# Performance work log

Measured on AMD Instinct MI355X. Metric: run time of the kernel, lower is better.

The kernel has to match this reference:

```python
import jax, jax.numpy as jnp
import numpy as np

LMAX, RB, RA, N, D = 4, 12, 11, 131072, 64
S = (LMAX + 1) ** 2


def _assoc_legendre_norm(lmax, x):
    # Fully-normalized associated Legendre P_l^m(x), orthonormal over the sphere
    # (includes sqrt((2l+1)/(4pi) * (l-m)!/(l+m)!)). x: [B] = cos(beta).
    B = x.shape[0]
    s = np.sqrt(np.clip(1.0 - x * x, 0.0, 1.0))
    P = np.zeros((lmax + 1, lmax + 1, B))
    P[0, 0] = np.sqrt(1.0 / (4.0 * np.pi))
    for m in range(1, lmax + 1):
        P[m, m] = -np.sqrt((2.0 * m + 1.0) / (2.0 * m)) * s * P[m - 1, m - 1]
    for m in range(0, lmax):
        P[m + 1, m] = np.sqrt(2.0 * m + 3.0) * x * P[m, m]
    for m in range(0, lmax + 1):
        for l in range(m + 2, lmax + 1):
            a = np.sqrt((4.0 * l * l - 1.0) / (l * l - m * m))
            b = np.sqrt((((l - 1) ** 2 - m * m)) / (4.0 * (l - 1) ** 2 - 1.0))
            P[l, m] = a * (x * P[l - 1, m] - b * P[l - 2, m])
    return P


def _sh_grid(lmax, res_beta, res_alpha):
    # Real orthonormal spherical harmonics sampled on a Gauss-Legendre x uniform-alpha grid,
    # plus quadrature weights so that sum_{b,a} Y_i Y_j qw_b = delta_ij (band-limited).
    x, w = np.polynomial.legendre.leggauss(res_beta)  # nodes in cos(beta)
    alpha = 2.0 * np.pi * np.arange(res_alpha) / res_alpha
    P = _assoc_legendre_norm(lmax, x)  # [L+1, L+1, RB]
    Ssz = (lmax + 1) ** 2
    Y = np.zeros((res_beta, res_alpha, Ssz))
    i = 0
    for l in range(lmax + 1):
        for m in range(-l, l + 1):
            if m < 0:
                ang = np.sqrt(2.0) * np.sin(-m * alpha)
            elif m == 0:
                ang = np.ones_like(alpha)
            else:
                ang = np.sqrt(2.0) * np.cos(m * alpha)
            Y[:, :, i] = P[l, abs(m)][:, None] * ang[None, :]
            i += 1
    qw = w * (2.0 * np.pi / res_alpha)  # beta quadrature * alpha trapezoid weight
    return Y.astype(np.float32), qw.astype(np.float32)


def setup_inputs() -> dict:
    key = jax.random.key(0)
    k1, k2, k3, k4 = jax.random.split(key, 4)
    Y_np, qw_np = _sh_grid(LMAX, RB, RA)
    Y = jnp.asarray(Y_np)                       # [RB, RA, S]
    Yw = Y * jnp.asarray(qw_np)[:, None, None]  # [RB, RA, S] (quadrature-weighted)
    input1 = jax.random.normal(k1, (N, D), dtype=jnp.float32)
    input2 = jax.random.normal(k2, (N, D), dtype=jnp.float32)
    W1 = jax.random.normal(k3, (D, S), dtype=jnp.float32) * 0.1
    W2 = jax.random.normal(k4, (D, S), dtype=jnp.float32) * 0.1
    return {"input1": input1, "input2": input2, "W1": W1, "W2": W2, "Y": Y, "Yw": Yw}


def reference(input1, input2, W1, W2, Y, Yw):
    # linear_in: project input irreps to S2 spherical-harmonic coefficients
    c1 = input1 @ W1  # [N, S]
    c2 = input2 @ W2  # [N, S]
    # ToS2Grid: evaluate band-limited signal on the (beta, alpha) grid
    g1 = jnp.einsum("ns,bas->nba", c1, Y)  # [N, RB, RA]
    g2 = jnp.einsum("ns,bas->nba", c2, Y)
    # pointwise product on the sphere, then FromS2Grid (quadrature projection)
    return jnp.einsum("nba,bas->ns", g1 * g2, Yw)  # [N, S]
```

## Files before the change

kernel.cpp:

```cpp
#include <hip/hip_runtime.h>


typedef __bf16 bf16x8 __attribute__((ext_vector_type(8)));
typedef float f32x4 __attribute__((ext_vector_type(4)));

namespace {
constexpr int kD = 64, kS = 25, kP = 132;
constexpr int kBlock = 256, kM = 128;
constexpr int kHStride = 168;
constexpr int kSmemU = kM * kHStride;
constexpr int kWsA2 = 9216, kWsB2 = 18432;
}

__device__ __forceinline__ unsigned short f2bf(float f) {
    unsigned int u = __builtin_bit_cast(unsigned int, f);
    u += 0x7FFFu + ((u >> 16) & 1u);
    return (unsigned short)(u >> 16);
}

__device__ __forceinline__ bf16x8 ld_frag_g(const unsigned short* p) {
    int4 v = *reinterpret_cast<const int4*>(p);
    return __builtin_bit_cast(bf16x8, v);
}

__device__ __forceinline__ bf16x8 cvt8(f32x4 u, f32x4 v) {
    bf16x8 r;
    r[0] = (__bf16)u[0]; r[1] = (__bf16)u[1]; r[2] = (__bf16)u[2]; r[3] = (__bf16)u[3];
    r[4] = (__bf16)v[0]; r[5] = (__bf16)v[1]; r[6] = (__bf16)v[2]; r[7] = (__bf16)v[3];
    return r;
}

__global__ void precompute_kernel(const float* __restrict__ W1,
                                  const float* __restrict__ W2,
                                  const float* __restrict__ Y,
                                  const float* __restrict__ Yw,
                                  unsigned short* __restrict__ ws) {
    const int t0 = blockIdx.x * blockDim.x + threadIdx.x;
    const int stride = gridDim.x * blockDim.x;
    for (int e = t0; e < 9216; e += stride) {
        const int j = e & 7, lane = (e >> 3) & 63, ks = (e >> 9) & 1, nt = e >> 10;
        const int k = ks * 32 + (lane >> 4) * 8 + j;
        const int n = nt * 16 + (lane & 15);
        float v1 = 0.f, v2 = 0.f;
        if (n < kP) {
            const float* yr = Y + n * kS;
            const float* w1 = W1 + k * kS;
            const float* w2 = W2 + k * kS;
            #pragma unroll
            for (int s = 0; s < kS; ++s) {
                v1 = fmaf(w1[s], yr[s], v1);
                v2 = fmaf(w2[s], yr[s], v2);
            }
        }
        ws[e]         = f2bf(v1);
        ws[kWsA2 + e] = f2bf(v2);
    }
    for (int e = t0; e < 5120; e += stride) {
        const int j = e & 7, lane = (e >> 3) & 63, r = e >> 9;
        const int ks = r % 5, nt = r / 5;
        const int k = ks * 32 + (lane >> 4) * 8 + j;
        const int n = nt * 16 + (lane & 15);
        ws[kWsB2 + e] = (k < kP && n < kS) ? f2bf(Yw[k * kS + n]) : (unsigned short)0;
    }
}

__global__ __launch_bounds__(kBlock, 3) void gaunt_mfma5(
    const float* __restrict__ in1, const float* __restrict__ in2,
    const unsigned short* __restrict__ ws, float* __restrict__ out)
{
    __shared__ unsigned short smem[kSmemU];
    const int tid  = threadIdx.x;
    const int lane = tid & 63;
    const int w    = __builtin_amdgcn_readfirstlane(tid >> 6);
    const int lo16 = lane & 15, quad = lane >> 4;

    {
        const int r = tid >> 1, c = 144 + (tid & 1) * 8;
        *reinterpret_cast<int4*>(&smem[r * kHStride + c]) = (int4){0, 0, 0, 0};
    }

    const long long base = (long long)blockIdx.x * (kM * kD);
    bf16x8 a1f[2][2], a2f[2][2];
    #pragma unroll
    for (int rt = 0; rt < 2; ++rt) {
        const int row = (2 * w + rt) * 16 + lo16;
        const float* p1 = in1 + base + row * kD + quad * 8;
        const float* p2 = in2 + base + row * kD + quad * 8;
        #pragma unroll
        for (int ks = 0; ks < 2; ++ks) {
            const f32x4 u1 = *reinterpret_cast<const f32x4*>(p1 + ks * 32);
            const f32x4 v1 = *reinterpret_cast<const f32x4*>(p1 + ks * 32 + 4);
            const f32x4 u2 = *reinterpret_cast<const f32x4*>(p2 + ks * 32);
            const f32x4 v2 = *reinterpret_cast<const f32x4*>(p2 + ks * 32 + 4);
            a1f[rt][ks] = cvt8(u1, v1);
            a2f[rt][ks] = cvt8(u2, v2);
        }
    }

    const unsigned short* wsA1 = ws;
    const unsigned short* wsA2 = ws + kWsA2;
    bf16x8 b1c[2], b2c[2], b1n[2], b2n[2];
    #pragma unroll
    for (int ks = 0; ks < 2; ++ks) {
        b1c[ks] = ld_frag_g(&wsA1[ks * 512 + lane * 8]);
        b2c[ks] = ld_frag_g(&wsA2[ks * 512 + lane * 8]);
    }
    #pragma unroll 1
    for (int nt = 0; nt < 9; ++nt) {
        if (nt < 8) {
            #pragma unroll
            for (int ks = 0; ks < 2; ++ks) {
                b1n[ks] = ld_frag_g(&wsA1[((nt + 1) * 2 + ks) * 512 + lane * 8]);
                b2n[ks] = ld_frag_g(&wsA2[((nt + 1) * 2 + ks) * 512 + lane * 8]);
            }
        }
        #pragma unroll
        for (int rt = 0; rt < 2; ++rt) {
            f32x4 g1 = (f32x4){0.f, 0.f, 0.f, 0.f};
            f32x4 g2 = (f32x4){0.f, 0.f, 0.f, 0.f};
            #pragma unroll
            for (int ks = 0; ks < 2; ++ks) {
                g1 = __builtin_amdgcn_mfma_f32_16x16x32_bf16(a1f[rt][ks], b1c[ks], g1, 0, 0, 0);
                g2 = __builtin_amdgcn_mfma_f32_16x16x32_bf16(a2f[rt][ks], b2c[ks], g2, 0, 0, 0);
            }
            const int hcol = nt * 16 + lo16;
            #pragma unroll
            for (int i = 0; i < 4; ++i) {
                const int row = (2 * w + rt) * 16 + quad * 4 + i;
                smem[row * kHStride + hcol] =
                    __builtin_bit_cast(unsigned short, (__bf16)(g1[i] * g2[i]));
            }
        }
        #pragma unroll
        for (int ks = 0; ks < 2; ++ks) { b1c[ks] = b1n[ks]; b2c[ks] = b2n[ks]; }
    }

    const unsigned short* wsB2 = ws + kWsB2;
    f32x4 o[2][2];
    #pragma unroll
    for (int rt = 0; rt < 2; ++rt)
        #pragma unroll
        for (int nt = 0; nt < 2; ++nt)
            o[rt][nt] = (f32x4){0.f, 0.f, 0.f, 0.f};

    bf16x8 bbc[2], bbn[2];
    #pragma unroll
    for (int nt = 0; nt < 2; ++nt)
        bbc[nt] = ld_frag_g(&wsB2[(nt * 5) * 512 + lane * 8]);

    #pragma unroll 1
    for (int ks = 0; ks < 5; ++ks) {
        if (ks < 4) {
            #pragma unroll
            for (int nt = 0; nt < 2; ++nt)
                bbn[nt] = ld_frag_g(&wsB2[(nt * 5 + ks + 1) * 512 + lane * 8]);
        }
        bf16x8 hf[2];
        #pragma unroll
        for (int rt = 0; rt < 2; ++rt) {
            const int row = (2 * w + rt) * 16 + lo16;
            const int4 hv = *reinterpret_cast<const int4*>(
                &smem[row * kHStride + ks * 32 + quad * 8]);
            hf[rt] = __builtin_bit_cast(bf16x8, hv);
        }
        #pragma unroll
        for (int rt = 0; rt < 2; ++rt)
            #pragma unroll
            for (int nt = 0; nt < 2; ++nt)
                o[rt][nt] = __builtin_amdgcn_mfma_f32_16x16x32_bf16(
                    hf[rt], bbc[nt], o[rt][nt], 0, 0, 0);
        bbc[0] = bbn[0]; bbc[1] = bbn[1];
    }

    const long long ob = (long long)blockIdx.x * (kM * kS);
    #pragma unroll
    for (int rt = 0; rt < 2; ++rt) {
        #pragma unroll
        for (int nt = 0; nt < 2; ++nt) {
            const int col = nt * 16 + lo16;
            if (col < kS) {
                #pragma unroll
                for (int i = 0; i < 4; ++i) {
                    const int row = (2 * w + rt) * 16 + quad * 4 + i;
                    out[ob + row * kS + col] = o[rt][nt][i];
                }
            }
        }
    }
}

extern "C" void kernel_launch(void* const* d_in, const int* in_sizes, int n_in,
                              void* d_out, int out_size, void* d_ws, size_t ws_size,
                              hipStream_t stream) {
    const float* in1 = (const float*)d_in[0];
    const float* in2 = (const float*)d_in[1];
    const float* W1  = (const float*)d_in[2];
    const float* W2  = (const float*)d_in[3];
    const float* Y   = (const float*)d_in[4];
    const float* Yw  = (const float*)d_in[5];
    float* out = (float*)d_out;
    unsigned short* ws = (unsigned short*)d_ws;

    precompute_kernel<<<8, 256, 0, stream>>>(W1, W2, Y, Yw, ws);

    const int n_rows = in_sizes[0] / kD;
    const int grid = n_rows / kM;
    gaunt_mfma5<<<grid, kBlock, 0, stream>>>(in1, in2, ws, out);
}
```

Before: 118.0 us.

## Fuse grid product into projection MFMA via register transpose, drop LDS staging

The first GEMMs are computed transposed, with the grid points as rows and the sample rows as columns. The product g1*g2 therefore lands in registers already laid out as the B operand of a 16x16x16 f16 MFMA. That second projection now accumulates inside the same loop, removing the shared-memory buffer, its stores and loads, and the separate second phase. Precision moves from bf16 to fp16, occupancy hint rises to 4 blocks, and output stores are vectorized, at some risk of fp16 overflow or range issues.

```diff
diff --git a/kernel.cpp b/kernel.cpp
--- a/kernel.cpp
+++ b/kernel.cpp
@@ -1,86 +1,78 @@
 #include <hip/hip_runtime.h>
 
 
-typedef __bf16 bf16x8 __attribute__((ext_vector_type(8)));
+typedef _Float16 f16x8 __attribute__((ext_vector_type(8)));
+typedef _Float16 f16x4 __attribute__((ext_vector_type(4)));
 typedef float f32x4 __attribute__((ext_vector_type(4)));
+typedef float f32x4u __attribute__((ext_vector_type(4), aligned(4)));
 
 namespace {
 constexpr int kD = 64, kS = 25, kP = 132;
 constexpr int kBlock = 256, kM = 128;
-constexpr int kHStride = 168;
-constexpr int kSmemU = kM * kHStride;
-constexpr int kWsA2 = 9216, kWsB2 = 18432;
-}
-
-__device__ __forceinline__ unsigned short f2bf(float f) {
-    unsigned int u = __builtin_bit_cast(unsigned int, f);
-    u += 0x7FFFu + ((u >> 16) & 1u);
-    return (unsigned short)(u >> 16);
-}
-
-__device__ __forceinline__ bf16x8 ld_frag_g(const unsigned short* p) {
-    int4 v = *reinterpret_cast<const int4*>(p);
-    return __builtin_bit_cast(bf16x8, v);
-}
-
-__device__ __forceinline__ bf16x8 cvt8(f32x4 u, f32x4 v) {
-    bf16x8 r;
-    r[0] = (__bf16)u[0]; r[1] = (__bf16)u[1]; r[2] = (__bf16)u[2]; r[3] = (__bf16)u[3];
-    r[4] = (__bf16)v[0]; r[5] = (__bf16)v[1]; r[6] = (__bf16)v[2]; r[7] = (__bf16)v[3];
-    return r;
+constexpr int kWsA2 = 9216, kWsYw = 18432;
 }
 
 __global__ void precompute_kernel(const float* __restrict__ W1,
                                   const float* __restrict__ W2,
                                   const float* __restrict__ Y,
                                   const float* __restrict__ Yw,
-                                  unsigned short* __restrict__ ws) {
+                                  _Float16* __restrict__ ws) {
     const int t0 = blockIdx.x * blockDim.x + threadIdx.x;
     const int stride = gridDim.x * blockDim.x;
     for (int e = t0; e < 9216; e += stride) {
-        const int j = e & 7, lane = (e >> 3) & 63, ks = (e >> 9) & 1, nt = e >> 10;
-        const int k = ks * 32 + (lane >> 4) * 8 + j;
-        const int n = nt * 16 + (lane & 15);
+        const int j = e & 7, lane = (e >> 3) & 63, ks = (e >> 9) & 1, pt = e >> 10;
+        const int d = ks * 32 + (lane >> 4) * 8 + j;
+        const int p = pt * 16 + (lane & 15);
         float v1 = 0.f, v2 = 0.f;
-        if (n < kP) {
-            const float* yr = Y + n * kS;
-            const float* w1 = W1 + k * kS;
-            const float* w2 = W2 + k * kS;
+        if (p < kP) {
+            const float* yr = Y + p * kS;
+            const float* w1 = W1 + d * kS;
+            const float* w2 = W2 + d * kS;
             #pragma unroll
             for (int s = 0; s < kS; ++s) {
                 v1 = fmaf(w1[s], yr[s], v1);
                 v2 = fmaf(w2[s], yr[s], v2);
             }
         }
-        ws[e]         = f2bf(v1);
-        ws[kWsA2 + e] = f2bf(v2);
+        ws[e]         = (_Float16)v1;
+        ws[kWsA2 + e] = (_Float16)v2;
     }
-    for (int e = t0; e < 5120; e += stride) {
-        const int j = e & 7, lane = (e >> 3) & 63, r = e >> 9;
-        const int ks = r % 5, nt = r / 5;
-        const int k = ks * 32 + (lane >> 4) * 8 + j;
-        const int n = nt * 16 + (lane & 15);
-        ws[kWsB2 + e] = (k < kP && n < kS) ? f2bf(Yw[k * kS + n]) : (unsigned short)0;
+    for (int e = t0; e < 4608; e += stride) {
+        const int i = e & 3, lane = (e >> 2) & 63, r = e >> 8;
+        const int pt = r % 9, st = r / 9;
+        const int p = pt * 16 + ((lane >> 4) & 3) * 4 + i;
+        const int s = st * 16 + (lane & 15);
+        ws[kWsYw + e] = (s < kS && p < kP) ? (_Float16)Yw[p * kS + s]
+                                           : (_Float16)0.f;
     }
 }
 
-__global__ __launch_bounds__(kBlock, 3) void gaunt_mfma5(
+__device__ __forceinline__ f16x8 ld8(const _Float16* p) {
+    return *reinterpret_cast<const f16x8*>(p);
+}
+__device__ __forceinline__ f16x4 ld4(const _Float16* p) {
+    return *reinterpret_cast<const f16x4*>(p);
+}
+__device__ __forceinline__ f16x8 cvt8h(f32x4 u, f32x4 v) {
+    f16x8 r;
+    r[0] = (_Float16)u[0]; r[1] = (_Float16)u[1];
+    r[2] = (_Float16)u[2]; r[3] = (_Float16)u[3];
+    r[4] = (_Float16)v[0]; r[5] = (_Float16)v[1];
+    r[6] = (_Float16)v[2]; r[7] = (_Float16)v[3];
+    return r;
+}
+
+__global__ __launch_bounds__(kBlock, 4) void gaunt_mfma6(
     const float* __restrict__ in1, const float* __restrict__ in2,
-    const unsigned short* __restrict__ ws, float* __restrict__ out)
+    const _Float16* __restrict__ ws, float* __restrict__ out)
 {
-    __shared__ unsigned short smem[kSmemU];
     const int tid  = threadIdx.x;
     const int lane = tid & 63;
     const int w    = __builtin_amdgcn_readfirstlane(tid >> 6);
     const int lo16 = lane & 15, quad = lane >> 4;
 
-    {
-        const int r = tid >> 1, c = 144 + (tid & 1) * 8;
-        *reinterpret_cast<int4*>(&smem[r * kHStride + c]) = (int4){0, 0, 0, 0};
-    }
-
     const long long base = (long long)blockIdx.x * (kM * kD);
-    bf16x8 a1f[2][2], a2f[2][2];
+    f16x8 b1[2][2], b2[2][2];
     #pragma unroll
     for (int rt = 0; rt < 2; ++rt) {
         const int row = (2 * w + rt) * 16 + lo16;
@@ -92,27 +84,44 @@
             const f32x4 v1 = *reinterpret_cast<const f32x4*>(p1 + ks * 32 + 4);
             const f32x4 u2 = *reinterpret_cast<const f32x4*>(p2 + ks * 32);
             const f32x4 v2 = *reinterpret_cast<const f32x4*>(p2 + ks * 32 + 4);
-            a1f[rt][ks] = cvt8(u1, v1);
-            a2f[rt][ks] = cvt8(u2, v2);
+            b1[rt][ks] = cvt8h(u1, v1);
+            b2[rt][ks] = cvt8h(u2, v2);
         }
     }
 
-    const unsigned short* wsA1 = ws;
-    const unsigned short* wsA2 = ws + kWsA2;
-    bf16x8 b1c[2], b2c[2], b1n[2], b2n[2];
+    const _Float16* wsA1 = ws;
+    const _Float16* wsA2 = ws + kWsA2;
+    const _Float16* wsYw = ws + kWsYw;
+
+    f32x4 oacc[2][2];
+    #pragma unroll
+    for (int rt = 0; rt < 2; ++rt)
+        #pragma unroll
+        for (int st = 0; st < 2; ++st)
+            oacc[rt][st] = (f32x4){0.f, 0.f, 0.f, 0.f};
+
+    f16x8 a1c[2], a2c[2], a1n[2], a2n[2];
+    f16x4 ywc[2], ywn[2];
     #pragma unroll
     for (int ks = 0; ks < 2; ++ks) {
-        b1c[ks] = ld_frag_g(&wsA1[ks * 512 + lane * 8]);
-        b2c[ks] = ld_frag_g(&wsA2[ks * 512 + lane * 8]);
+        a1c[ks] = ld8(&wsA1[ks * 512 + lane * 8]);
+        a2c[ks] = ld8(&wsA2[ks * 512 + lane * 8]);
     }
+    #pragma unroll
+    for (int st = 0; st < 2; ++st)
+        ywc[st] = ld4(&wsYw[(st * 9) * 256 + lane * 4]);
+
     #pragma unroll 1
-    for (int nt = 0; nt < 9; ++nt) {
-        if (nt < 8) {
+    for (int pt = 0; pt < 9; ++pt) {
+        if (pt < 8) {
             #pragma unroll
             for (int ks = 0; ks < 2; ++ks) {
-                b1n[ks] = ld_frag_g(&wsA1[((nt + 1) * 2 + ks) * 512 + lane * 8]);
-                b2n[ks] = ld_frag_g(&wsA2[((nt + 1) * 2 + ks) * 512 + lane * 8]);
+                a1n[ks] = ld8(&wsA1[((pt + 1) * 2 + ks) * 512 + lane * 8]);
+                a2n[ks] = ld8(&wsA2[((pt + 1) * 2 + ks) * 512 + lane * 8]);
             }
+            #pragma unroll
+            for (int st = 0; st < 2; ++st)
+                ywn[st] = ld4(&wsYw[(st * 9 + pt + 1) * 256 + lane * 4]);
         }
         #pragma unroll
         for (int rt = 0; rt < 2; ++rt) {
@@ -120,71 +129,34 @@
             f32x4 g2 = (f32x4){0.f, 0.f, 0.f, 0.f};
             #pragma unroll
             for (int ks = 0; ks < 2; ++ks) {
-                g1 = __builtin_amdgcn_mfma_f32_16x16x32_bf16(a1f[rt][ks], b1c[ks], g1, 0, 0, 0);
-                g2 = __builtin_amdgcn_mfma_f32_16x16x32_bf16(a2f[rt][ks], b2c[ks], g2, 0, 0, 0);
+                g1 = __builtin_amdgcn_mfma_f32_16x16x32_f16(a1c[ks], b1[rt][ks], g1, 0, 0, 0);
+                g2 = __builtin_amdgcn_mfma_f32_16x16x32_f16(a2c[ks], b2[rt][ks], g2, 0, 0, 0);
             }
-            const int hcol = nt * 16 + lo16;
+            f16x4 h;
+            h[0] = (_Float16)(g1[0] * g2[0]);
+            h[1] = (_Float16)(g1[1] * g2[1]);
+            h[2] = (_Float16)(g1[2] * g2[2]);
+            h[3] = (_Float16)(g1[3] * g2[3]);
             #pragma unroll
-            for (int i = 0; i < 4; ++i) {
-                const int row = (2 * w + rt) * 16 + quad * 4 + i;
-                smem[row * kHStride + hcol] =
-                    __builtin_bit_cast(unsigned short, (__bf16)(g1[i] * g2[i]));
-            }
+            for (int st = 0; st < 2; ++st)
+                oacc[rt][st] = __builtin_amdgcn_mfma_f32_16x16x16f16(
+                    ywc[st], h, oacc[rt][st], 0, 0, 0);
         }
         #pragma unroll
-        for (int ks = 0; ks < 2; ++ks) { b1c[ks] = b1n[ks]; b2c[ks] = b2n[ks]; }
-    }
-
-    const unsigned short* wsB2 = ws + kWsB2;
-    f32x4 o[2][2];
-    #pragma unroll
-    for (int rt = 0; rt < 2; ++rt)
-        #pragma unroll
-        for (int nt = 0; nt < 2; ++nt)
-            o[rt][nt] = (f32x4){0.f, 0.f, 0.f, 0.f};
-
-    bf16x8 bbc[2], bbn[2];
-    #pragma unroll
-    for (int nt = 0; nt < 2; ++nt)
-        bbc[nt] = ld_frag_g(&wsB2[(nt * 5) * 512 + lane * 8]);
-
-    #pragma unroll 1
-    for (int ks = 0; ks < 5; ++ks) {
-        if (ks < 4) {
-            #pragma unroll
-            for (int nt = 0; nt < 2; ++nt)
-                bbn[nt] = ld_frag_g(&wsB2[(nt * 5 + ks + 1) * 512 + lane * 8]);
-        }
-        bf16x8 hf[2];
-        #pragma unroll
-        for (int rt = 0; rt < 2; ++rt) {
-            const int row = (2 * w + rt) * 16 + lo16;
-            const int4 hv = *reinterpret_cast<const int4*>(
-                &smem[row * kHStride + ks * 32 + quad * 8]);
-            hf[rt] = __builtin_bit_cast(bf16x8, hv);
-        }
-        #pragma unroll
-        for (int rt = 0; rt < 2; ++rt)
-            #pragma unroll
-            for (int nt = 0; nt < 2; ++nt)
-                o[rt][nt] = __builtin_amdgcn_mfma_f32_16x16x32_bf16(
-                    hf[rt], bbc[nt], o[rt][nt], 0, 0, 0);
-        bbc[0] = bbn[0]; bbc[1] = bbn[1];
+        for (int ks = 0; ks < 2; ++ks) { a1c[ks] = a1n[ks]; a2c[ks] = a2n[ks]; }
+        ywc[0] = ywn[0]; ywc[1] = ywn[1];
     }
 
     const long long ob = (long long)blockIdx.x * (kM * kS);
     #pragma unroll
     for (int rt = 0; rt < 2; ++rt) {
-        #pragma unroll
-        for (int nt = 0; nt < 2; ++nt) {
-            const int col = nt * 16 + lo16;
-            if (col < kS) {
-                #pragma unroll
-                for (int i = 0; i < 4; ++i) {
-                    const int row = (2 * w + rt) * 16 + quad * 4 + i;
-                    out[ob + row * kS + col] = o[rt][nt][i];
-                }
-            }
+        const int row = (2 * w + rt) * 16 + lo16;
+        float* rp = out + ob + (long long)row * kS;
+        *reinterpret_cast<f32x4u*>(rp + quad * 4) = oacc[rt][0];
+        if (quad < 2) {
+            *reinterpret_cast<f32x4u*>(rp + 16 + quad * 4) = oacc[rt][1];
+        } else if (quad == 2) {
+            rp[24] = oacc[rt][1][0];
         }
     }
 }
@@ -199,11 +171,11 @@
     const float* Y   = (const float*)d_in[4];
     const float* Yw  = (const float*)d_in[5];
     float* out = (float*)d_out;
-    unsigned short* ws = (unsigned short*)d_ws;
+    _Float16* ws = (_Float16*)d_ws;
 
-    precompute_kernel<<<8, 256, 0, stream>>>(W1, W2, Y, Yw, ws);
+    precompute_kernel<<<16, 256, 0, stream>>>(W1, W2, Y, Yw, ws);
 
     const int n_rows = in_sizes[0] / kD;
     const int grid = n_rows / kM;
-    gaunt_mfma5<<<grid, kBlock, 0, stream>>>(in1, in2, ws, out);
+    gaunt_mfma6<<<grid, kBlock, 0, stream>>>(in1, in2, ws, out);
 }
```

After: 117.0 us. No clear change (-0.8%).
